# Kernel optimization log

Measured on AMD Instinct MI355X. Metric: run time of the kernel, lower is better.

The kernel has to match this reference:

```python
import jax, jax.numpy as jnp
import numpy as np

B, T, C = 4, 4096, 256
H = 4
D = C // H
EPS = 1e-5


def layer_norm(x, w, b):
    mean = x.mean(axis=-1, keepdims=True)
    var = x.var(axis=-1, keepdims=True)
    return w * (x - mean) / jnp.sqrt(var + EPS) + b


def setup_inputs() -> dict:
    key = jax.random.key(0)
    ks = jax.random.split(key, 8)
    s = lambda n: 1.0 / np.sqrt(n)
    return {
        "x": jax.random.normal(ks[0], (B, T, C), jnp.float32),
        "qkv_w": jax.random.normal(ks[1], (C, 3 * C), jnp.float32) * s(C),
        "qkv_b": jnp.zeros((3 * C,), jnp.float32),
        "proj_w": jax.random.normal(ks[2], (C, C), jnp.float32) * s(C),
        "proj_b": jnp.zeros((C,), jnp.float32),
        "n1_w": jnp.ones((C,), jnp.float32),
        "n1_b": jnp.zeros((C,), jnp.float32),
        "ffn_w1": jax.random.normal(ks[3], (C, 3 * C), jnp.float32) * s(C),
        "ffn_b1": jnp.zeros((3 * C,), jnp.float32),
        "ffn_w2": jax.random.normal(ks[4], (3 * C, C), jnp.float32) * s(3 * C),
        "ffn_b2": jnp.zeros((C,), jnp.float32),
        "n2_w": jnp.ones((C,), jnp.float32),
        "n2_b": jnp.zeros((C,), jnp.float32),
    }


def reference(x, qkv_w, qkv_b, proj_w, proj_b, n1_w, n1_b,
              ffn_w1, ffn_b1, ffn_w2, ffn_b2, n2_w, n2_b):
    scale = D ** -0.5
    qkv = (x @ qkv_w + qkv_b).reshape(B, T, 3, H, D)
    qkv = jnp.transpose(qkv, (2, 0, 3, 1, 4))  # [3, B, H, T, D]
    q, k, v = qkv[0], qkv[1], qkv[2]
    attn = jnp.einsum('bhtd,bhsd->bhts', q, k) * scale  # [B,H,T,T]
    attn = jax.nn.softmax(attn, axis=-1)
    out = jnp.einsum('bhts,bhsd->bhtd', attn, v)
    out = jnp.transpose(out, (0, 2, 1, 3)).reshape(B, T, C)
    attn_out = out @ proj_w + proj_b
    x = layer_norm(x + attn_out, n1_w, n1_b)
    h = jax.nn.gelu(x @ ffn_w1 + ffn_b1, approximate=False)
    ffn_out = h @ ffn_w2 + ffn_b2
    x = layer_norm(x + ffn_out, n2_w, n2_b)
    return x
```

## Files before the change

kernel.cpp:

```cpp
#include <hip/hip_runtime.h>
#include <cstdint>
#include <cstddef>

typedef __bf16 bf16;
typedef __bf16 bf16x8 __attribute__((ext_vector_type(8)));
typedef __bf16 bf16x4 __attribute__((ext_vector_type(4)));
typedef _Float16 f16;
typedef _Float16 f16x4 __attribute__((ext_vector_type(4)));
typedef _Float16 f16x8 __attribute__((ext_vector_type(8)));
typedef __fp16 fp16x2 __attribute__((ext_vector_type(2)));
typedef float f32x4 __attribute__((ext_vector_type(4)));

#define DEV static __device__ __forceinline__
#if __has_builtin(__builtin_amdgcn_exp2f)
#define EXP2(x) __builtin_amdgcn_exp2f(x)
#else
#define EXP2(x) exp2f(x)
#endif
#define QSCALE 0.18033688011112042f

DEV float gelu_exact(float v) {
  return 0.5f * v * (1.0f + erff(v * 0.70710678118654752f));
}

__global__ void cvt_w_kernel(const float* __restrict__ qkv_w, bf16* __restrict__ qwt,
                             const float* __restrict__ proj_w, bf16* __restrict__ pwt,
                             const float* __restrict__ f1w, bf16* __restrict__ f1wt,
                             const float* __restrict__ f2w, bf16* __restrict__ f2wt) {
  int blk = blockIdx.x;
  const float* w; bf16* o; int K, N;
  if (blk < 48)       { w = qkv_w;  o = qwt;  K = 256; N = 768; }
  else if (blk < 64)  { w = proj_w; o = pwt;  K = 256; N = 256; blk -= 48; }
  else if (blk < 112) { w = f1w;    o = f1wt; K = 256; N = 768; blk -= 64; }
  else                { w = f2w;    o = f2wt; K = 768; N = 256; blk -= 112; }
  const int ntiles = N >> 6;
  const int kt = blk / ntiles, nt = blk - kt * ntiles;
  const int k0 = kt * 64, n0 = nt * 64;
  __shared__ float tile[64][65];
  const int tid = threadIdx.x;
#pragma unroll
  for (int j = 0; j < 4; ++j) {
    const int c = j * 256 + tid;
    const int row = c >> 4, c4 = (c & 15) * 4;
    const float4 v = *(const float4*)(w + (size_t)(k0 + row) * N + n0 + c4);
    tile[row][c4] = v.x; tile[row][c4 + 1] = v.y;
    tile[row][c4 + 2] = v.z; tile[row][c4 + 3] = v.w;
  }
  __syncthreads();
#pragma unroll
  for (int j = 0; j < 4; ++j) {
    const int c = j * 256 + tid;
    const int n = c >> 4, k4 = (c & 15) * 4;
    bf16x4 ov;
#pragma unroll
    for (int i = 0; i < 4; ++i) ov[i] = (bf16)tile[k4 + i][n];
    *(bf16x4*)(o + (size_t)(n0 + n) * K + k0 + k4) = ov;
  }
}

__global__ __launch_bounds__(256, 2)
void gemm_qkv_kernel(const float* __restrict__ A, const bf16* __restrict__ Wt,
                     const float* __restrict__ bias, bf16* __restrict__ qb,
                     bf16* __restrict__ kb, f16* __restrict__ vt) {
  const int tid = threadIdx.x;
  const int wave = tid >> 6, lane = tid & 63;
  const int quad = lane >> 4, l15 = lane & 15;
  const int m0 = blockIdx.y * 128, n0 = blockIdx.x * 128;
  const int mw = (wave >> 1) * 64, nw = (wave & 1) * 64;
  const int K = 256;

  __shared__ bf16 lA[128 * 72];
  __shared__ bf16 lB[128 * 72];

  f32x4 acc[4][4] = {};

  for (int k0 = 0; k0 < K; k0 += 64) {
#pragma unroll
    for (int j = 0; j < 4; ++j) {
      const int c = j * 256 + tid;
      const int row = c >> 3, kc = (c & 7) * 8;
      const float* ax = A + (size_t)(m0 + row) * K + k0 + kc;
      const float4 a0 = *(const float4*)(ax);
      const float4 a1 = *(const float4*)(ax + 4);
      bf16x8 ab;
      ab[0] = (bf16)a0.x; ab[1] = (bf16)a0.y; ab[2] = (bf16)a0.z; ab[3] = (bf16)a0.w;
      ab[4] = (bf16)a1.x; ab[5] = (bf16)a1.y; ab[6] = (bf16)a1.z; ab[7] = (bf16)a1.w;
      *(bf16x8*)(lA + row * 72 + kc) = ab;
      *(uint4*)(lB + row * 72 + kc) =
          *(const uint4*)(Wt + (size_t)(n0 + row) * K + k0 + kc);
    }
    __syncthreads();
#pragma unroll
    for (int ks = 0; ks < 2; ++ks) {
      bf16x8 af[4], bfm[4];
#pragma unroll
      for (int i = 0; i < 4; ++i)
        af[i] = *(const bf16x8*)(lA + (mw + i * 16 + l15) * 72 + ks * 32 + quad * 8);
#pragma unroll
      for (int j = 0; j < 4; ++j)
        bfm[j] = *(const bf16x8*)(lB + (nw + j * 16 + l15) * 72 + ks * 32 + quad * 8);
#pragma unroll
      for (int i = 0; i < 4; ++i)
#pragma unroll
        for (int j = 0; j < 4; ++j)
          acc[i][j] = __builtin_amdgcn_mfma_f32_16x16x32_bf16(af[i], bfm[j],
                                                              acc[i][j], 0, 0, 0);
    }
    __syncthreads();
  }

  const bool isV = (n0 >= 512);
#pragma unroll
  for (int i = 0; i < 4; ++i) {
#pragma unroll
    for (int j = 0; j < 4; ++j) {
      const int n = n0 + nw + j * 16 + l15;
      const float bs = bias[n];
      if (isV) {
        const int m = m0 + mw + i * 16 + quad * 4;
        const int b = m >> 12, t = m & 4095;
        const int h = (n >> 6) & 3, d = n & 63;
        const int tp = (t & ~31) | (((t >> 2) & 3) << 3) | (((t >> 4) & 1) << 2);
        f16x4 hv;
#pragma unroll
        for (int r = 0; r < 4; ++r) hv[r] = (f16)(acc[i][j][r] + bs);
        *(f16x4*)(vt + (size_t)((b * 4 + h) * 64 + d) * 4096 + tp) = hv;
      } else {
        const int s = n >> 8, cc = n & 255, h = cc >> 6, d = cc & 63;
#pragma unroll
        for (int r = 0; r < 4; ++r) {
          const int m = m0 + mw + i * 16 + quad * 4 + r;
          const int b = m >> 12, t = m & 4095;
          const float v = acc[i][j][r] + bs;
          const size_t idx = (size_t)((b * 4 + h) * 4096 + t) * 64 + d;
          if (s == 0) qb[idx] = (bf16)(v * QSCALE);
          else        kb[idx] = (bf16)v;
        }
      }
    }
  }
}

__global__ __launch_bounds__(256, 2)
void attn_kernel(const bf16* __restrict__ q, const bf16* __restrict__ k,
                 const f16* __restrict__ vt, bf16* __restrict__ o) {
  const int tid = threadIdx.x;
  const int wave = tid >> 6, lane = tid & 63;
  const int quad = lane >> 4, l15 = lane & 15;
  const int bh = blockIdx.y;
  const int q0 = blockIdx.x * 128;
  __shared__ bf16 lK[2][64 * 72];
  __shared__ f16  lV[2][64 * 72];

  bf16x8 qa0[2], qa1[2];
#pragma unroll
  for (int s = 0; s < 2; ++s) {
    const bf16* qp =
        q + ((size_t)bh * 4096 + q0 + wave * 32 + s * 16 + l15) * 64 + quad * 8;
    qa0[s] = *(const bf16x8*)(qp);
    qa1[s] = *(const bf16x8*)(qp + 32);
  }

  const int row0 = tid >> 3, off = (tid & 7) * 8;
  const bf16* kp = k + ((size_t)bh * 4096 + row0) * 64 + off;
  const f16*  vp = vt + ((size_t)bh * 64 + row0) * 4096 + off;
  const int lidx = row0 * 72 + off;

  *(uint4*)(lK[0] + lidx)            = *(const uint4*)(kp);
  *(uint4*)(lK[0] + lidx + 32 * 72)  = *(const uint4*)(kp + 32 * 64);
  *(uint4*)(lV[0] + lidx)            = *(const uint4*)(vp);
  *(uint4*)(lV[0] + lidx + 32 * 72)  = *(const uint4*)(vp + 32 * 4096);

  f32x4 accO[2][4] = {};
  f32x4 accD[2] = {};
  const f16x8 vone8 = {(f16)1.0f, (f16)1.0f, (f16)1.0f, (f16)1.0f,
                       (f16)1.0f, (f16)1.0f, (f16)1.0f, (f16)1.0f};
  uint4 pk0, pk1, pv0, pv1;

  for (int it = 0; it < 64; ++it) {
    const int cur = it & 1;
    if (it + 1 < 64) {
      const bf16* kn = kp + (size_t)(it + 1) * 64 * 64;
      const f16*  vn = vp + (it + 1) * 64;
      pk0 = *(const uint4*)(kn);
      pk1 = *(const uint4*)(kn + 32 * 64);
      pv0 = *(const uint4*)(vn);
      pv1 = *(const uint4*)(vn + 32 * 4096);
    }
    __syncthreads();

    f32x4 sf[2][4];
#pragma unroll
    for (int c = 0; c < 4; ++c) {
      const bf16x8 kb0 = *(const bf16x8*)(lK[cur] + (c * 16 + l15) * 72 + quad * 8);
      const bf16x8 kb1 = *(const bf16x8*)(lK[cur] + (c * 16 + l15) * 72 + 32 + quad * 8);
#pragma unroll
      for (int s = 0; s < 2; ++s) {
        f32x4 t = {};
        t = __builtin_amdgcn_mfma_f32_16x16x32_bf16(kb0, qa0[s], t, 0, 0, 0);
        t = __builtin_amdgcn_mfma_f32_16x16x32_bf16(kb1, qa1[s], t, 0, 0, 0);
        sf[s][c] = t;
      }
    }

    f16x8 pa[2][2];
#pragma unroll
    for (int s = 0; s < 2; ++s)
#pragma unroll
      for (int c2 = 0; c2 < 2; ++c2) {
        union { fp16x2 h2[4]; f16x8 h8; } u;
        u.h2[0] = __builtin_amdgcn_cvt_pkrtz(EXP2(sf[s][2 * c2][0]),
                                             EXP2(sf[s][2 * c2][1]));
        u.h2[1] = __builtin_amdgcn_cvt_pkrtz(EXP2(sf[s][2 * c2][2]),
                                             EXP2(sf[s][2 * c2][3]));
        u.h2[2] = __builtin_amdgcn_cvt_pkrtz(EXP2(sf[s][2 * c2 + 1][0]),
                                             EXP2(sf[s][2 * c2 + 1][1]));
        u.h2[3] = __builtin_amdgcn_cvt_pkrtz(EXP2(sf[s][2 * c2 + 1][2]),
                                             EXP2(sf[s][2 * c2 + 1][3]));
        pa[s][c2] = u.h8;
      }

#pragma unroll
    for (int s = 0; s < 2; ++s)
#pragma unroll
      for (int c2 = 0; c2 < 2; ++c2)
        accD[s] = __builtin_amdgcn_mfma_f32_16x16x32_f16(pa[s][c2], vone8,
                                                         accD[s], 0, 0, 0);

#pragma unroll
    for (int c2 = 0; c2 < 2; ++c2) {
#pragma unroll
      for (int n = 0; n < 4; ++n) {
        const f16x8 vb =
            *(const f16x8*)(lV[cur] + (n * 16 + l15) * 72 + c2 * 32 + quad * 8);
#pragma unroll
        for (int s = 0; s < 2; ++s)
          accO[s][n] = __builtin_amdgcn_mfma_f32_16x16x32_f16(pa[s][c2], vb,
                                                              accO[s][n], 0, 0, 0);
      }
    }

    if (it + 1 < 64) {
      *(uint4*)(lK[cur ^ 1] + lidx)           = pk0;
      *(uint4*)(lK[cur ^ 1] + lidx + 32 * 72) = pk1;
      *(uint4*)(lV[cur ^ 1] + lidx)           = pv0;
      *(uint4*)(lV[cur ^ 1] + lidx + 32 * 72) = pv1;
    }
  }

  const int b = bh >> 2, h = bh & 3;
#pragma unroll
  for (int s = 0; s < 2; ++s) {
    float inv[4];
#pragma unroll
    for (int r = 0; r < 4; ++r) inv[r] = 1.0f / accD[s][r];
#pragma unroll
    for (int n = 0; n < 4; ++n)
#pragma unroll
      for (int r = 0; r < 4; ++r) {
        const int t = q0 + wave * 32 + s * 16 + quad * 4 + r;
        o[(size_t)(b * 4096 + t) * 256 + h * 64 + n * 16 + l15] =
            (bf16)(accO[s][n][r] * inv[r]);
      }
  }
}

__global__ __launch_bounds__(256, 2)
void gemm_ffn1_kernel(const bf16* __restrict__ A, const bf16* __restrict__ Wt,
                      const float* __restrict__ bias, bf16* __restrict__ ob) {
  const int tid = threadIdx.x;
  const int wave = tid >> 6, lane = tid & 63;
  const int quad = lane >> 4, l15 = lane & 15;
  const int m0 = blockIdx.y * 128, n0 = blockIdx.x * 128;
  const int mw = (wave >> 1) * 64, nw = (wave & 1) * 64;
  const int K = 256;

  __shared__ bf16 lA[128 * 72];
  __shared__ bf16 lB[128 * 72];

  f32x4 acc[4][4] = {};

  for (int k0 = 0; k0 < K; k0 += 64) {
#pragma unroll
    for (int j = 0; j < 4; ++j) {
      const int c = j * 256 + tid;
      const int row = c >> 3, kc = (c & 7) * 8;
      *(uint4*)(lA + row * 72 + kc) =
          *(const uint4*)(A + (size_t)(m0 + row) * K + k0 + kc);
      *(uint4*)(lB + row * 72 + kc) =
          *(const uint4*)(Wt + (size_t)(n0 + row) * K + k0 + kc);
    }
    __syncthreads();
#pragma unroll
    for (int ks = 0; ks < 2; ++ks) {
      bf16x8 af[4], bfm[4];
#pragma unroll
      for (int i = 0; i < 4; ++i)
        af[i] = *(const bf16x8*)(lA + (mw + i * 16 + l15) * 72 + ks * 32 + quad * 8);
#pragma unroll
      for (int j = 0; j < 4; ++j)
        bfm[j] = *(const bf16x8*)(lB + (nw + j * 16 + l15) * 72 + ks * 32 + quad * 8);
#pragma unroll
      for (int i = 0; i < 4; ++i)
#pragma unroll
        for (int j = 0; j < 4; ++j)
          acc[i][j] = __builtin_amdgcn_mfma_f32_16x16x32_bf16(af[i], bfm[j],
                                                              acc[i][j], 0, 0, 0);
    }
    __syncthreads();
  }

#pragma unroll
  for (int i = 0; i < 4; ++i) {
#pragma unroll
    for (int j = 0; j < 4; ++j) {
      const int n = n0 + nw + j * 16 + l15;
      const float bs = bias[n];
#pragma unroll
      for (int r = 0; r < 4; ++r) {
        const int m = m0 + mw + i * 16 + quad * 4 + r;
        ob[(size_t)m * 768 + n] = (bf16)gelu_exact(acc[i][j][r] + bs);
      }
    }
  }
}

template <int KTILES, bool RESID_BF16, bool WRITE_F, bool WRITE_B>
__global__ __launch_bounds__(256, 3)
void gemm_ln_kernel(const bf16* __restrict__ A, const bf16* __restrict__ Wt,
                    const float* __restrict__ bias, const void* __restrict__ Rv,
                    const float* __restrict__ lw, const float* __restrict__ lb,
                    float* __restrict__ outf, bf16* __restrict__ outb) {
  const int tid = threadIdx.x;
  const int wave = tid >> 6, lane = tid & 63;
  const int quad = lane >> 4, l15 = lane & 15;
  const int m0 = blockIdx.x * 32;
  const int nw = wave * 64;
  const int K = KTILES * 64;
  __shared__ bf16 lA[32 * 72];
  __shared__ bf16 lB[256 * 72];
  __shared__ float lnsum[4][32];
  __shared__ float lnsq[4][32];
  __shared__ float lnstat[32][2];
  f32x4 acc[2][4] = {};

  for (int kt = 0; kt < KTILES; ++kt) {
    const int k0 = kt * 64;
    {
      const int row = tid >> 3, kc = (tid & 7) * 8;
      *(uint4*)(lA + row * 72 + kc) =
          *(const uint4*)(A + (size_t)(m0 + row) * K + k0 + kc);
    }
#pragma unroll
    for (int j = 0; j < 8; ++j) {
      const int c = j * 256 + tid;
      const int row = c >> 3, kc = (c & 7) * 8;
      *(uint4*)(lB + row * 72 + kc) =
          *(const uint4*)(Wt + (size_t)row * K + k0 + kc);
    }
    __syncthreads();
#pragma unroll
    for (int ks = 0; ks < 2; ++ks) {
      bf16x8 af[2], bfm[4];
#pragma unroll
      for (int i = 0; i < 2; ++i)
        af[i] = *(const bf16x8*)(lA + (i * 16 + l15) * 72 + ks * 32 + quad * 8);
#pragma unroll
      for (int j = 0; j < 4; ++j)
        bfm[j] = *(const bf16x8*)(lB + (nw + j * 16 + l15) * 72 + ks * 32 + quad * 8);
#pragma unroll
      for (int i = 0; i < 2; ++i)
#pragma unroll
        for (int j = 0; j < 4; ++j)
          acc[i][j] = __builtin_amdgcn_mfma_f32_16x16x32_bf16(af[i], bfm[j],
                                                              acc[i][j], 0, 0, 0);
    }
    __syncthreads();
  }

  float bv[4], lwv[4], lbv[4];
#pragma unroll
  for (int j = 0; j < 4; ++j) {
    const int col = nw + 16 * j + l15;
    bv[j] = bias[col]; lwv[j] = lw[col]; lbv[j] = lb[col];
  }
#pragma unroll
  for (int i = 0; i < 2; ++i) {
    float ps[4] = {}, pq[4] = {};
#pragma unroll
    for (int j = 0; j < 4; ++j) {
#pragma unroll
      for (int r = 0; r < 4; ++r) {
        const int m = m0 + 16 * i + 4 * quad + r;
        const size_t ri = (size_t)m * 256 + nw + 16 * j + l15;
        const float rv = RESID_BF16 ? (float)((const bf16*)Rv)[ri]
                                    : ((const float*)Rv)[ri];
        const float v = acc[i][j][r] + bv[j] + rv;
        acc[i][j][r] = v;
        ps[r] += v;
        pq[r] += v * v;
      }
    }
#pragma unroll
    for (int r = 0; r < 4; ++r) {
#pragma unroll
      for (int mm = 1; mm < 16; mm <<= 1) {
        ps[r] += __shfl_xor(ps[r], mm, 64);
        pq[r] += __shfl_xor(pq[r], mm, 64);
      }
      if (l15 == 0) {
        lnsum[wave][16 * i + 4 * quad + r] = ps[r];
        lnsq[wave][16 * i + 4 * quad + r] = pq[r];
      }
    }
  }
  __syncthreads();
  if (tid < 32) {
    const float s = lnsum[0][tid] + lnsum[1][tid] + lnsum[2][tid] + lnsum[3][tid];
    const float sq = lnsq[0][tid] + lnsq[1][tid] + lnsq[2][tid] + lnsq[3][tid];
    const float mean = s * (1.0f / 256.0f);
    const float var = sq * (1.0f / 256.0f) - mean * mean;
    lnstat[tid][0] = mean;
    lnstat[tid][1] = rsqrtf(var + 1e-5f);
  }
  __syncthreads();
#pragma unroll
  for (int i = 0; i < 2; ++i) {
#pragma unroll
    for (int r = 0; r < 4; ++r) {
      const int row = 16 * i + 4 * quad + r;
      const float mean = lnstat[row][0], rstd = lnstat[row][1];
#pragma unroll
      for (int j = 0; j < 4; ++j) {
        const float ov = (acc[i][j][r] - mean) * rstd * lwv[j] + lbv[j];
        const size_t gi = (size_t)(m0 + row) * 256 + nw + 16 * j + l15;
        if constexpr (WRITE_F) outf[gi] = ov;
        if constexpr (WRITE_B) outb[gi] = (bf16)ov;
      }
    }
  }
}

extern "C" void kernel_launch(void* const* d_in, const int* in_sizes, int n_in,
                              void* d_out, int out_size, void* d_ws, size_t ws_size,
                              hipStream_t stream) {
  const float* x      = (const float*)d_in[0];
  const float* qkv_w  = (const float*)d_in[1];
  const float* qkv_b  = (const float*)d_in[2];
  const float* proj_w = (const float*)d_in[3];
  const float* proj_b = (const float*)d_in[4];
  const float* n1_w   = (const float*)d_in[5];
  const float* n1_b   = (const float*)d_in[6];
  const float* ffn_w1 = (const float*)d_in[7];
  const float* ffn_b1 = (const float*)d_in[8];
  const float* ffn_w2 = (const float*)d_in[9];
  const float* ffn_b2 = (const float*)d_in[10];
  const float* n2_w   = (const float*)d_in[11];
  const float* n2_b   = (const float*)d_in[12];
  float* out = (float*)d_out;

  char* ws = (char*)d_ws;
  bf16*  qwt  = (bf16*)(ws + 0);
  bf16*  pwt  = (bf16*)(ws + 393216);
  bf16*  f1wt = (bf16*)(ws + 524288);
  bf16*  f2wt = (bf16*)(ws + 917504);
  bf16*  qb   = (bf16*)(ws + 1310720);
  bf16*  kb   = (bf16*)(ws + 9699328);
  f16*   vtb  = (f16*)(ws + 18087936);
  bf16*  attn = (bf16*)(ws + 26476544);
  bf16*  x1b  = (bf16*)(ws + 34865152);
  bf16*  hbuf = (bf16*)(ws + 1310720);

  cvt_w_kernel<<<160, 256, 0, stream>>>(qkv_w, qwt, proj_w, pwt,
                                        ffn_w1, f1wt, ffn_w2, f2wt);
  gemm_qkv_kernel<<<dim3(6, 128), 256, 0, stream>>>(x, qwt, qkv_b, qb, kb, vtb);
  attn_kernel<<<dim3(32, 16), 256, 0, stream>>>(qb, kb, vtb, attn);
  gemm_ln_kernel<4, false, false, true><<<512, 256, 0, stream>>>(
      attn, pwt, proj_b, x, n1_w, n1_b, nullptr, x1b);
  gemm_ffn1_kernel<<<dim3(6, 128), 256, 0, stream>>>(x1b, f1wt, ffn_b1, hbuf);
  gemm_ln_kernel<12, true, true, false><<<512, 256, 0, stream>>>(
      hbuf, f2wt, ffn_b2, x1b, n2_w, n2_b, out, nullptr);
}
```

Baseline: 238.1 us.

## Split attention over KV halves, pre-convert x to bf16, add setprio

The attention kernel now splits the key/value range into two halves along a new grid dimension. Each half writes its partial normalized output and its softmax denominator, and a new combine kernel merges them weighted by the denominators. Input x is converted to bf16 inside the weight-conversion kernel, so the QKV GEMM loads bf16 directly. Launch bounds for the GEMMs rise to 3 blocks per CU, and the MFMA sections get s_setprio hints. This doubles attention parallelism (512 to 1024 blocks) at the cost of an extra kernel, extra memory traffic, and bf16 rounding of the partial outputs.

```diff
diff --git a/kernel.cpp b/kernel.cpp
--- a/kernel.cpp
+++ b/kernel.cpp
@@ -26,8 +26,20 @@
 __global__ void cvt_w_kernel(const float* __restrict__ qkv_w, bf16* __restrict__ qwt,
                              const float* __restrict__ proj_w, bf16* __restrict__ pwt,
                              const float* __restrict__ f1w, bf16* __restrict__ f1wt,
-                             const float* __restrict__ f2w, bf16* __restrict__ f2wt) {
+                             const float* __restrict__ f2w, bf16* __restrict__ f2wt,
+                             const float* __restrict__ x, bf16* __restrict__ xb) {
   int blk = blockIdx.x;
+  const int tid = threadIdx.x;
+  if (blk >= 160) {
+    const size_t i = ((size_t)(blk - 160) * 256 + tid) * 8;
+    const float4 a0 = *(const float4*)(x + i);
+    const float4 a1 = *(const float4*)(x + i + 4);
+    bf16x8 v;
+    v[0] = (bf16)a0.x; v[1] = (bf16)a0.y; v[2] = (bf16)a0.z; v[3] = (bf16)a0.w;
+    v[4] = (bf16)a1.x; v[5] = (bf16)a1.y; v[6] = (bf16)a1.z; v[7] = (bf16)a1.w;
+    *(bf16x8*)(xb + i) = v;
+    return;
+  }
   const float* w; bf16* o; int K, N;
   if (blk < 48)       { w = qkv_w;  o = qwt;  K = 256; N = 768; }
   else if (blk < 64)  { w = proj_w; o = pwt;  K = 256; N = 256; blk -= 48; }
@@ -37,7 +49,6 @@
   const int kt = blk / ntiles, nt = blk - kt * ntiles;
   const int k0 = kt * 64, n0 = nt * 64;
   __shared__ float tile[64][65];
-  const int tid = threadIdx.x;
 #pragma unroll
   for (int j = 0; j < 4; ++j) {
     const int c = j * 256 + tid;
@@ -58,8 +69,8 @@
   }
 }
 
-__global__ __launch_bounds__(256, 2)
-void gemm_qkv_kernel(const float* __restrict__ A, const bf16* __restrict__ Wt,
+__global__ __launch_bounds__(256, 3)
+void gemm_qkv_kernel(const bf16* __restrict__ A, const bf16* __restrict__ Wt,
                      const float* __restrict__ bias, bf16* __restrict__ qb,
                      bf16* __restrict__ kb, f16* __restrict__ vt) {
   const int tid = threadIdx.x;
@@ -79,13 +90,8 @@
     for (int j = 0; j < 4; ++j) {
       const int c = j * 256 + tid;
       const int row = c >> 3, kc = (c & 7) * 8;
-      const float* ax = A + (size_t)(m0 + row) * K + k0 + kc;
-      const float4 a0 = *(const float4*)(ax);
-      const float4 a1 = *(const float4*)(ax + 4);
-      bf16x8 ab;
-      ab[0] = (bf16)a0.x; ab[1] = (bf16)a0.y; ab[2] = (bf16)a0.z; ab[3] = (bf16)a0.w;
-      ab[4] = (bf16)a1.x; ab[5] = (bf16)a1.y; ab[6] = (bf16)a1.z; ab[7] = (bf16)a1.w;
-      *(bf16x8*)(lA + row * 72 + kc) = ab;
+      *(uint4*)(lA + row * 72 + kc) =
+          *(const uint4*)(A + (size_t)(m0 + row) * K + k0 + kc);
       *(uint4*)(lB + row * 72 + kc) =
           *(const uint4*)(Wt + (size_t)(n0 + row) * K + k0 + kc);
     }
@@ -143,12 +149,15 @@
 
 __global__ __launch_bounds__(256, 2)
 void attn_kernel(const bf16* __restrict__ q, const bf16* __restrict__ k,
-                 const f16* __restrict__ vt, bf16* __restrict__ o) {
+                 const f16* __restrict__ vt, bf16* __restrict__ o0,
+                 bf16* __restrict__ o1, float* __restrict__ pD) {
   const int tid = threadIdx.x;
   const int wave = tid >> 6, lane = tid & 63;
   const int quad = lane >> 4, l15 = lane & 15;
   const int bh = blockIdx.y;
   const int q0 = blockIdx.x * 128;
+  const int z = blockIdx.z;
+  const int kvbase = z * 2048;
   __shared__ bf16 lK[2][64 * 72];
   __shared__ f16  lV[2][64 * 72];
 
@@ -162,8 +171,8 @@
   }
 
   const int row0 = tid >> 3, off = (tid & 7) * 8;
-  const bf16* kp = k + ((size_t)bh * 4096 + row0) * 64 + off;
-  const f16*  vp = vt + ((size_t)bh * 64 + row0) * 4096 + off;
+  const bf16* kp = k + ((size_t)bh * 4096 + kvbase + row0) * 64 + off;
+  const f16*  vp = vt + ((size_t)bh * 64 + row0) * 4096 + kvbase + off;
   const int lidx = row0 * 72 + off;
 
   *(uint4*)(lK[0] + lidx)            = *(const uint4*)(kp);
@@ -177,9 +186,9 @@
                        (f16)1.0f, (f16)1.0f, (f16)1.0f, (f16)1.0f};
   uint4 pk0, pk1, pv0, pv1;
 
-  for (int it = 0; it < 64; ++it) {
+  for (int it = 0; it < 32; ++it) {
     const int cur = it & 1;
-    if (it + 1 < 64) {
+    if (it + 1 < 32) {
       const bf16* kn = kp + (size_t)(it + 1) * 64 * 64;
       const f16*  vn = vp + (it + 1) * 64;
       pk0 = *(const uint4*)(kn);
@@ -190,6 +199,7 @@
     __syncthreads();
 
     f32x4 sf[2][4];
+    __builtin_amdgcn_s_setprio(1);
 #pragma unroll
     for (int c = 0; c < 4; ++c) {
       const bf16x8 kb0 = *(const bf16x8*)(lK[cur] + (c * 16 + l15) * 72 + quad * 8);
@@ -202,6 +212,7 @@
         sf[s][c] = t;
       }
     }
+    __builtin_amdgcn_s_setprio(0);
 
     f16x8 pa[2][2];
 #pragma unroll
@@ -220,6 +231,7 @@
         pa[s][c2] = u.h8;
       }
 
+    __builtin_amdgcn_s_setprio(1);
 #pragma unroll
     for (int s = 0; s < 2; ++s)
 #pragma unroll
@@ -239,8 +251,9 @@
                                                               accO[s][n], 0, 0, 0);
       }
     }
-
-    if (it + 1 < 64) {
+    __builtin_amdgcn_s_setprio(0);
+
+    if (it + 1 < 32) {
       *(uint4*)(lK[cur ^ 1] + lidx)           = pk0;
       *(uint4*)(lK[cur ^ 1] + lidx + 32 * 72) = pk1;
       *(uint4*)(lV[cur ^ 1] + lidx)           = pv0;
@@ -248,6 +261,7 @@
     }
   }
 
+  bf16* po = z ? o1 : o0;
   const int b = bh >> 2, h = bh & 3;
 #pragma unroll
   for (int s = 0; s < 2; ++s) {
@@ -255,17 +269,38 @@
 #pragma unroll
     for (int r = 0; r < 4; ++r) inv[r] = 1.0f / accD[s][r];
 #pragma unroll
-    for (int n = 0; n < 4; ++n)
-#pragma unroll
-      for (int r = 0; r < 4; ++r) {
-        const int t = q0 + wave * 32 + s * 16 + quad * 4 + r;
-        o[(size_t)(b * 4096 + t) * 256 + h * 64 + n * 16 + l15] =
+    for (int r = 0; r < 4; ++r) {
+      const int t = q0 + wave * 32 + s * 16 + quad * 4 + r;
+      if (l15 == 0) pD[(size_t)(z * 16 + bh) * 4096 + t] = accD[s][r];
+#pragma unroll
+      for (int n = 0; n < 4; ++n)
+        po[(size_t)(b * 4096 + t) * 256 + h * 64 + n * 16 + l15] =
             (bf16)(accO[s][n][r] * inv[r]);
-      }
-  }
-}
-
-__global__ __launch_bounds__(256, 2)
+    }
+  }
+}
+
+__global__ __launch_bounds__(256)
+void attn_combine_kernel(bf16* __restrict__ o0, const bf16* __restrict__ o1,
+                         const float* __restrict__ pD) {
+  const size_t base = ((size_t)blockIdx.x * 256 + threadIdx.x) * 8;
+  const int row = (int)(base >> 8);
+  const int b = row >> 12, t = row & 4095;
+  const int h = ((int)(base >> 6)) & 3;
+  const float d0 = pD[(size_t)(b * 4 + h) * 4096 + t];
+  const float d1 = pD[(size_t)(16 + b * 4 + h) * 4096 + t];
+  const float w = 1.0f / (d0 + d1);
+  const float w0 = d0 * w, w1 = d1 * w;
+  const bf16x8 a = *(const bf16x8*)(o0 + base);
+  const bf16x8 c = *(const bf16x8*)(o1 + base);
+  bf16x8 r;
+#pragma unroll
+  for (int i = 0; i < 8; ++i)
+    r[i] = (bf16)((float)a[i] * w0 + (float)c[i] * w1);
+  *(bf16x8*)(o0 + base) = r;
+}
+
+__global__ __launch_bounds__(256, 3)
 void gemm_ffn1_kernel(const bf16* __restrict__ A, const bf16* __restrict__ Wt,
                       const float* __restrict__ bias, bf16* __restrict__ ob) {
   const int tid = threadIdx.x;
@@ -470,11 +505,15 @@
   bf16*  attn = (bf16*)(ws + 26476544);
   bf16*  x1b  = (bf16*)(ws + 34865152);
   bf16*  hbuf = (bf16*)(ws + 1310720);
-
-  cvt_w_kernel<<<160, 256, 0, stream>>>(qkv_w, qwt, proj_w, pwt,
-                                        ffn_w1, f1wt, ffn_w2, f2wt);
-  gemm_qkv_kernel<<<dim3(6, 128), 256, 0, stream>>>(x, qwt, qkv_b, qb, kb, vtb);
-  attn_kernel<<<dim3(32, 16), 256, 0, stream>>>(qb, kb, vtb, attn);
+  bf16*  xb   = (bf16*)(ws + 34865152);
+  bf16*  po1  = (bf16*)(ws + 34865152);
+  float* pden = (float*)(ws + 43253760);
+
+  cvt_w_kernel<<<2208, 256, 0, stream>>>(qkv_w, qwt, proj_w, pwt,
+                                         ffn_w1, f1wt, ffn_w2, f2wt, x, xb);
+  gemm_qkv_kernel<<<dim3(6, 128), 256, 0, stream>>>(xb, qwt, qkv_b, qb, kb, vtb);
+  attn_kernel<<<dim3(32, 16, 2), 256, 0, stream>>>(qb, kb, vtb, attn, po1, pden);
+  attn_combine_kernel<<<2048, 256, 0, stream>>>(attn, po1, pden);
   gemm_ln_kernel<4, false, false, true><<<512, 256, 0, stream>>>(
       attn, pwt, proj_b, x, n1_w, n1_b, nullptr, x1b);
   gemm_ffn1_kernel<<<dim3(6, 128), 256, 0, stream>>>(x1b, f1wt, ffn_b1, hbuf);
```

New measurement: 241.6 us. About the same (+1.5%).
